# Kernel tuning notes

Measured on AMD Instinct MI355X. Metric: run time of the kernel, lower is better.

Reference implementation:

```python
import jax, jax.numpy as jnp
import numpy as np

EPS = 1e-06


def rotation_trick(e, q):
    # e, q: (..., D). Faithful to torch version, but r_rT @ e and
    # q_hat_e_hatT @ e are algebraically simplified to r*(r.e) and
    # q_hat*(e_hat.e), avoiding the (..., D, D) outer-product tensors.
    sg = jax.lax.stop_gradient
    e_norm = sg(jnp.linalg.norm(e, axis=-1, keepdims=True)) + EPS
    q_norm = sg(jnp.linalg.norm(q, axis=-1, keepdims=True)) + EPS
    e_hat = sg(e / e_norm)
    q_hat = sg(q / q_norm)
    lmbda = q_norm / e_norm
    r = e_hat + q_hat
    r = r / jnp.linalg.norm(r, axis=-1, keepdims=True)
    r_dot_e = jnp.sum(r * e, axis=-1, keepdims=True)
    ehat_dot_e = jnp.sum(e_hat * e, axis=-1, keepdims=True)
    return lmbda * (e - 2.0 * r * r_dot_e + 2.0 * q_hat * ehat_dot_e)


def setup_inputs() -> dict:
    key = jax.random.key(0)
    k1, k2 = jax.random.split(key)
    B, D, H, W = 8, 64, 32, 32
    K = 8192
    x = jax.random.normal(k1, (B, D, H, W), dtype=jnp.float32)
    # init_tensor: L2-normalize uniform rand along dim=1, scale=1
    e = jax.random.uniform(k2, (D, K), dtype=jnp.float32)
    e_i_ts = e / (jnp.linalg.norm(e, axis=1, keepdims=True) + 1e-12)
    return {"x": x, "e_i_ts": e_i_ts}


def reference(x, e_i_ts):
    # x: (B, D, H, W); e_i_ts: (D, K)
    B, D, H, W = x.shape
    x_perm = jnp.transpose(x, (0, 2, 3, 1))          # (B, H, W, D)
    flat_x = x_perm.reshape(-1, D)                   # (N, D)
    distances = (
        jnp.sum(flat_x**2, axis=1, keepdims=True)
        - 2.0 * flat_x @ e_i_ts
        + jnp.sum(e_i_ts**2, axis=0, keepdims=True)
    )                                                # (N, K)
    encoding_indices = jnp.argmin(distances, axis=1) # (N,)
    ind = encoding_indices.reshape(B, H, W)
    quantized_x = e_i_ts.T[ind]                      # (B, H, W, D) gather
    quantized_x_d = rotation_trick(x_perm, quantized_x)
    # permute back to channels-first
    q = jnp.transpose(quantized_x, (0, 3, 1, 2))
    q_d = jnp.transpose(quantized_x_d, (0, 3, 1, 2))
    return (q_d, q, ind)
```

## Files before the change

kernel.cpp:

```cpp
#include <hip/hip_runtime.h>
#include <float.h>
#include <math.h>

#define EPS 1e-6f

typedef __attribute__((ext_vector_type(8))) short short8;
typedef __attribute__((ext_vector_type(4))) float f32x4;

constexpr int Nn = 8192;
constexpr int Dd = 64;
constexpr int Kk = 8192;
constexpr int PLANE = Nn * Dd;
constexpr int KSPLIT = 16;
constexpr int KPB = Kk / KSPLIT;
constexpr int NT = KPB / 16;
constexpr int NPAIR = NT / 2;
constexpr int TILE_USH = 4096;
constexpr int PAIR_BYTES = 2 * TILE_USH * 2;

__device__ __forceinline__ void split3(float v, unsigned short& h1, unsigned short& h2, unsigned short& h3) {
    unsigned u = __float_as_uint(v);
    h1 = (unsigned short)(u >> 16);
    float r1 = v - __uint_as_float((unsigned)h1 << 16);
    h2 = (unsigned short)(__float_as_uint(r1) >> 16);
    float r2 = r1 - __uint_as_float((unsigned)h2 << 16);
    h3 = (unsigned short)(__float_as_uint(r2) >> 16);
}

__device__ __forceinline__ unsigned sortable(float v) {
    unsigned u = __float_as_uint(v);
    return (u & 0x80000000u) ? ~u : (u | 0x80000000u);
}
__device__ __forceinline__ float unsortable(unsigned s) {
    unsigned u = (s & 0x80000000u) ? (s & 0x7FFFFFFFu) : ~s;
    return __uint_as_float(u);
}

typedef __attribute__((address_space(3))) unsigned int lds_u32_t;
typedef __attribute__((address_space(1))) unsigned int glb_u32_t;
__device__ __forceinline__ void gload_lds16(const void* g, void* l) {
    __builtin_amdgcn_global_load_lds((const glb_u32_t*)g, (lds_u32_t*)l, 16, 0, 0);
}

__global__ __launch_bounds__(128) void prep_kernel(
    const float* __restrict__ e, const float* __restrict__ x,
    unsigned short* __restrict__ es_t, float* __restrict__ en2h,
    float* __restrict__ et,
    unsigned short* __restrict__ xs, float* __restrict__ xn2,
    unsigned long long* __restrict__ packed)
{
    const int tid = threadIdx.x;
    if (blockIdx.x < 64) {
        const int k = blockIdx.x * 128 + tid;
        const int t = k >> 4, l15 = k & 15;
        unsigned short* tb = es_t + (size_t)t * TILE_USH;
        float s = 0.f;
        #pragma unroll
        for (int c = 0; c < 8; ++c) {
            const int ks = c >> 2, kg = c & 3;
            short8 h1v, h2v, h3v;
            float fv[8];
            #pragma unroll
            for (int j = 0; j < 8; ++j) {
                float v = e[(c * 8 + j) * Kk + k];
                fv[j] = v;
                s = fmaf(v, v, s);
                unsigned short h1, h2, h3; split3(v, h1, h2, h3);
                h1v[j] = (short)h1; h2v[j] = (short)h2; h3v[j] = (short)h3;
            }
            const int lofs = (kg * 16 + l15) * 8;
            *(short8*)(tb + (0 * 2 + ks) * 512 + lofs) = h1v;
            *(short8*)(tb + (1 * 2 + ks) * 512 + lofs) = h2v;
            *(short8*)(tb + (2 * 2 + ks) * 512 + lofs) = h3v;
            *(float4*)(et + (size_t)k * Dd + c * 8)     = *(float4*)&fv[0];
            *(float4*)(et + (size_t)k * Dd + c * 8 + 4) = *(float4*)&fv[4];
        }
        unsigned short s1, s2, s3; split3(0.5f * s, s1, s2, s3);
        short8 env = {(short)s1, (short)s2, (short)s3, 0, 0, 0, 0, 0};
        short8 zz  = {0, 0, 0, 0, 0, 0, 0, 0};
        *(short8*)(tb + 6 * 512 + l15 * 8) = env;
        *(short8*)(tb + 6 * 512 + (16 + l15) * 8) = zz;
        *(short8*)(tb + 6 * 512 + (32 + l15) * 8) = zz;
        *(short8*)(tb + 6 * 512 + (48 + l15) * 8) = zz;
        en2h[k] = 0.5f * s;
    } else {
        const int p = (blockIdx.x - 64) * 128 + tid;
        const int b = p >> 10, hw = p & 1023;
        packed[p] = ~0ull;
        float s = 0.f;
        #pragma unroll
        for (int c = 0; c < 8; ++c) {
            short8 h1v, h2v, h3v;
            #pragma unroll
            for (int j = 0; j < 8; ++j) {
                float v = x[(b * Dd + c * 8 + j) * 1024 + hw];
                s = fmaf(v, v, s);
                unsigned short h1, h2, h3; split3(-v, h1, h2, h3);
                h1v[j] = (short)h1; h2v[j] = (short)h2; h3v[j] = (short)h3;
            }
            *(short8*)(xs + (size_t)p * Dd + c * 8) = h1v;
            *(short8*)(xs + PLANE + (size_t)p * Dd + c * 8) = h2v;
            *(short8*)(xs + 2 * PLANE + (size_t)p * Dd + c * 8) = h3v;
        }
        xn2[p] = s;
    }
}

__device__ __forceinline__ void tile_compute(
    const short8 (&a)[2][3][2], const short8 a_ones, const short8 (&b)[7],
    int nb, int l15, float (&bv)[2][4], int (&bi)[2][4])
{
    const f32x4 zero = {0.f, 0.f, 0.f, 0.f};
    f32x4 acc_en = __builtin_amdgcn_mfma_f32_16x16x32_bf16(a_ones, b[6], zero, 0, 0, 0);
    f32x4 acc[2][2];
    acc[0][0] = acc_en; acc[1][0] = acc_en;
    acc[0][1] = zero;   acc[1][1] = zero;
    #define PROD(sx, se) \
        acc[0][0] = __builtin_amdgcn_mfma_f32_16x16x32_bf16(a[0][sx][0], b[(se)*2+0], acc[0][0], 0,0,0); \
        acc[1][0] = __builtin_amdgcn_mfma_f32_16x16x32_bf16(a[1][sx][0], b[(se)*2+0], acc[1][0], 0,0,0); \
        acc[0][1] = __builtin_amdgcn_mfma_f32_16x16x32_bf16(a[0][sx][1], b[(se)*2+1], acc[0][1], 0,0,0); \
        acc[1][1] = __builtin_amdgcn_mfma_f32_16x16x32_bf16(a[1][sx][1], b[(se)*2+1], acc[1][1], 0,0,0);
    PROD(0,0) PROD(0,1) PROD(1,0) PROD(0,2) PROD(1,1) PROD(2,0)
    #undef PROD
    #pragma unroll
    for (int mi = 0; mi < 2; ++mi)
        #pragma unroll
        for (int j = 0; j < 4; ++j) {
            float s = acc[mi][0][j] + acc[mi][1][j];
            if (s < bv[mi][j]) { bv[mi][j] = s; bi[mi][j] = nb + l15; }
        }
}

__global__ __launch_bounds__(256, 2) void dist_mfma(
    const unsigned short* __restrict__ xs, const unsigned short* __restrict__ es_t,
    unsigned long long* __restrict__ packed)
{
    __shared__ __align__(16) unsigned short sB[2][2 * TILE_USH];

    const int tid = threadIdx.x;
    const int w = tid >> 6, lane = tid & 63;
    const int l15 = lane & 15, kg = lane >> 4;
    const int m0 = blockIdx.x * 128 + w * 32;
    const int t0 = blockIdx.y * NT;
    const int pr0 = t0 / 2;

    short8 a[2][3][2];
    #pragma unroll
    for (int mi = 0; mi < 2; ++mi) {
        const unsigned short* xp = xs + (size_t)(m0 + mi * 16 + l15) * Dd + kg * 8;
        #pragma unroll
        for (int s = 0; s < 3; ++s)
            #pragma unroll
            for (int ks = 0; ks < 2; ++ks)
                a[mi][s][ks] = *(const short8*)(xp + s * PLANE + ks * 32);
    }
    const short8 a_ones = (kg == 0)
        ? short8{(short)0x3F80, (short)0x3F80, (short)0x3F80, 0, 0, 0, 0, 0}
        : short8{0, 0, 0, 0, 0, 0, 0, 0};

    float bv[2][4]; int bi[2][4];
    #pragma unroll
    for (int mi = 0; mi < 2; ++mi)
        #pragma unroll
        for (int j = 0; j < 4; ++j) { bv[mi][j] = FLT_MAX; bi[mi][j] = 0; }

    #define STAGE_PAIR(buf, pi) { \
        const char* gb_ = (const char*)es_t + (size_t)(pi) * PAIR_BYTES; \
        char* lb_ = (char*)&sB[buf][0]; \
        _Pragma("unroll") \
        for (int r_ = 0; r_ < 4; ++r_) { \
            const int off_ = r_ * 4096 + w * 1024; \
            gload_lds16(gb_ + off_ + lane * 16, lb_ + off_); } }

    STAGE_PAIR(0, pr0)
    asm volatile("s_waitcnt vmcnt(0)" ::: "memory");
    asm volatile("s_barrier" ::: "memory");

    #pragma unroll 1
    for (int pp = 0; pp < NPAIR; ++pp) {
        const int cur = pp & 1;
        const int pn = (pp + 1 < NPAIR) ? pp + 1 : NPAIR - 1;
        STAGE_PAIR(cur ^ 1, pr0 + pn)
        asm volatile("s_waitcnt vmcnt(4)" ::: "memory");
        asm volatile("s_barrier" ::: "memory");

        short8 bf0[7], bf1[7];
        const unsigned short* lb = &sB[cur][lane * 8];
        #pragma unroll
        for (int f = 0; f < 7; ++f) bf0[f] = *(const short8*)(lb + f * 512);
        #pragma unroll
        for (int f = 0; f < 7; ++f) bf1[f] = *(const short8*)(lb + TILE_USH + f * 512);
        asm volatile("s_waitcnt lgkmcnt(0)" ::: "memory");
        asm volatile("s_barrier" ::: "memory");

        const int ti = t0 + pp * 2;
        tile_compute(a, a_ones, bf0, ti * 16, l15, bv, bi);
        tile_compute(a, a_ones, bf1, ti * 16 + 16, l15, bv, bi);
    }

    #pragma unroll
    for (int m = 1; m < 16; m <<= 1) {
        #pragma unroll
        for (int mi = 0; mi < 2; ++mi)
            #pragma unroll
            for (int j = 0; j < 4; ++j) {
                float ov = __shfl_xor(bv[mi][j], m, 64);
                int   oi = __shfl_xor(bi[mi][j], m, 64);
                if (ov < bv[mi][j] || (ov == bv[mi][j] && oi < bi[mi][j])) {
                    bv[mi][j] = ov; bi[mi][j] = oi;
                }
            }
    }
    if (l15 == 0) {
        #pragma unroll
        for (int mi = 0; mi < 2; ++mi)
            #pragma unroll
            for (int j = 0; j < 4; ++j) {
                int pix = m0 + mi * 16 + kg * 4 + j;
                unsigned long long pk =
                    ((unsigned long long)sortable(bv[mi][j]) << 32) | (unsigned)bi[mi][j];
                atomicMin(&packed[pix], pk);
            }
    }
}

__global__ __launch_bounds__(256) void apply_kernel(
    const float* __restrict__ x, const float* __restrict__ et,
    const float* __restrict__ en2h, const float* __restrict__ xn2,
    const unsigned long long* __restrict__ packed,
    float* __restrict__ out_qd, float* __restrict__ out_q, float* __restrict__ out_ind)
{
    const int p = blockIdx.x * 256 + threadIdx.x;
    const unsigned long long pk = packed[p];
    const int bii = (int)(pk & 0xFFFFFFFFu);
    const float bvv = unsortable((unsigned)(pk >> 32));
    if (blockIdx.y == 0) out_ind[p] = (float)bii;

    float sx2 = xn2[p];
    float enh = en2h[bii];
    float sq2 = 2.f * enh;
    float sxq = enh - bvv;
    float ne = sqrtf(sx2), nq = sqrtf(sq2);
    float inv_e = 1.f / (ne + EPS), inv_q = 1.f / (nq + EPS);
    float lmbda = (nq + EPS) * inv_e;
    float ehat_dot_e = sx2 * inv_e;
    float rn2 = sx2 * inv_e * inv_e + 2.f * sxq * inv_e * inv_q + sq2 * inv_q * inv_q;
    float inv_r = rsqrtf(rn2);
    float rde = (sx2 * inv_e + sxq * inv_q) * inv_r;
    float cx = lmbda * (1.f - 2.f * rde * inv_r * inv_e);
    float cq = 2.f * lmbda * inv_q * (ehat_dot_e - rde * inv_r);

    const int b = p >> 10, hw = p & 1023;
    const int d0 = blockIdx.y * 8;
    const float* xb = x + (b * Dd + d0) * 1024 + hw;
    const float* er = et + (size_t)bii * Dd + d0;
    float* qd_b = out_qd + (b * Dd + d0) * 1024 + hw;
    float* q_b  = out_q  + (b * Dd + d0) * 1024 + hw;
    #pragma unroll
    for (int dv = 0; dv < 2; ++dv) {
        float4 q4 = *(const float4*)(er + dv * 4);
        #pragma unroll
        for (int jj = 0; jj < 4; ++jj) {
            int d = dv * 4 + jj;
            float xv = xb[d * 1024];
            float qv = ((const float*)&q4)[jj];
            qd_b[d * 1024] = cx * xv + cq * qv;
            q_b[d * 1024]  = qv;
        }
    }
}

extern "C" void kernel_launch(void* const* d_in, const int* in_sizes, int n_in,
                              void* d_out, int out_size, void* d_ws, size_t ws_size,
                              hipStream_t stream) {
    const float* x = (const float*)d_in[0];
    const float* e = (const float*)d_in[1];
    float* out = (float*)d_out;
    float* out_qd  = out;
    float* out_q   = out + Nn * Dd;
    float* out_ind = out + 2 * Nn * Dd;

    unsigned short* xs   = (unsigned short*)d_ws;
    unsigned short* es_t = xs + 3 * PLANE;
    float* et   = (float*)(es_t + (size_t)(Kk / 16) * TILE_USH);
    float* en2h = et + (size_t)Kk * Dd;
    float* xn2  = en2h + Kk;
    unsigned long long* packed = (unsigned long long*)(xn2 + Nn);

    prep_kernel<<<128, 128, 0, stream>>>(e, x, es_t, en2h, et, xs, xn2, packed);
    dist_mfma<<<dim3(Nn / 128, KSPLIT), 256, 0, stream>>>(xs, es_t, packed);
    apply_kernel<<<dim3(Nn / 256, 8), 256, 0, stream>>>(x, et, en2h, xn2, packed,
                                                        out_qd, out_q, out_ind);
}
```

Before: 61.27 us.

## Register-block four M tiles per wave with per-wave LDS staging and no barriers

```diff
diff --git a/kernel.cpp b/kernel.cpp
--- a/kernel.cpp
+++ b/kernel.cpp
@@ -14,9 +14,7 @@
 constexpr int KSPLIT = 16;
 constexpr int KPB = Kk / KSPLIT;
 constexpr int NT = KPB / 16;
-constexpr int NPAIR = NT / 2;
-constexpr int TILE_USH = 4096;
-constexpr int PAIR_BYTES = 2 * TILE_USH * 2;
+constexpr int TILE_USH = 3072;
 
 __device__ __forceinline__ void split3(float v, unsigned short& h1, unsigned short& h2, unsigned short& h3) {
     unsigned u = __float_as_uint(v);
@@ -75,13 +73,6 @@
             *(float4*)(et + (size_t)k * Dd + c * 8)     = *(float4*)&fv[0];
             *(float4*)(et + (size_t)k * Dd + c * 8 + 4) = *(float4*)&fv[4];
         }
-        unsigned short s1, s2, s3; split3(0.5f * s, s1, s2, s3);
-        short8 env = {(short)s1, (short)s2, (short)s3, 0, 0, 0, 0, 0};
-        short8 zz  = {0, 0, 0, 0, 0, 0, 0, 0};
-        *(short8*)(tb + 6 * 512 + l15 * 8) = env;
-        *(short8*)(tb + 6 * 512 + (16 + l15) * 8) = zz;
-        *(short8*)(tb + 6 * 512 + (32 + l15) * 8) = zz;
-        *(short8*)(tb + 6 * 512 + (48 + l15) * 8) = zz;
         en2h[k] = 0.5f * s;
     } else {
         const int p = (blockIdx.x - 64) * 128 + tid;
@@ -107,23 +98,25 @@
 }
 
 __device__ __forceinline__ void tile_compute(
-    const short8 (&a)[2][3][2], const short8 a_ones, const short8 (&b)[7],
-    int nb, int l15, float (&bv)[2][4], int (&bi)[2][4])
-{
-    const f32x4 zero = {0.f, 0.f, 0.f, 0.f};
-    f32x4 acc_en = __builtin_amdgcn_mfma_f32_16x16x32_bf16(a_ones, b[6], zero, 0, 0, 0);
-    f32x4 acc[2][2];
-    acc[0][0] = acc_en; acc[1][0] = acc_en;
-    acc[0][1] = zero;   acc[1][1] = zero;
+    const short8 (&a)[4][3][2], const short8 (&b)[6], float en,
+    int nb, int l15, float (&bv)[4][4], int (&bi)[4][4])
+{
+    f32x4 acc[4][2];
+    #pragma unroll
+    for (int mi = 0; mi < 4; ++mi) {
+        acc[mi][0] = f32x4{en, en, en, en};
+        acc[mi][1] = f32x4{0.f, 0.f, 0.f, 0.f};
+    }
     #define PROD(sx, se) \
-        acc[0][0] = __builtin_amdgcn_mfma_f32_16x16x32_bf16(a[0][sx][0], b[(se)*2+0], acc[0][0], 0,0,0); \
-        acc[1][0] = __builtin_amdgcn_mfma_f32_16x16x32_bf16(a[1][sx][0], b[(se)*2+0], acc[1][0], 0,0,0); \
-        acc[0][1] = __builtin_amdgcn_mfma_f32_16x16x32_bf16(a[0][sx][1], b[(se)*2+1], acc[0][1], 0,0,0); \
-        acc[1][1] = __builtin_amdgcn_mfma_f32_16x16x32_bf16(a[1][sx][1], b[(se)*2+1], acc[1][1], 0,0,0);
+        _Pragma("unroll") \
+        for (int mi = 0; mi < 4; ++mi) { \
+            acc[mi][0] = __builtin_amdgcn_mfma_f32_16x16x32_bf16(a[mi][sx][0], b[(se)*2+0], acc[mi][0], 0,0,0); \
+            acc[mi][1] = __builtin_amdgcn_mfma_f32_16x16x32_bf16(a[mi][sx][1], b[(se)*2+1], acc[mi][1], 0,0,0); \
+        }
     PROD(0,0) PROD(0,1) PROD(1,0) PROD(0,2) PROD(1,1) PROD(2,0)
     #undef PROD
     #pragma unroll
-    for (int mi = 0; mi < 2; ++mi)
+    for (int mi = 0; mi < 4; ++mi)
         #pragma unroll
         for (int j = 0; j < 4; ++j) {
             float s = acc[mi][0][j] + acc[mi][1][j];
@@ -131,22 +124,23 @@
         }
 }
 
-__global__ __launch_bounds__(256, 2) void dist_mfma(
+__global__ __launch_bounds__(256, 1) void dist_mfma(
     const unsigned short* __restrict__ xs, const unsigned short* __restrict__ es_t,
+    const float* __restrict__ en2h,
     unsigned long long* __restrict__ packed)
 {
-    __shared__ __align__(16) unsigned short sB[2][2 * TILE_USH];
+    __shared__ __align__(16) unsigned short sW[4][2][TILE_USH];
 
     const int tid = threadIdx.x;
     const int w = tid >> 6, lane = tid & 63;
     const int l15 = lane & 15, kg = lane >> 4;
-    const int m0 = blockIdx.x * 128 + w * 32;
-    const int t0 = blockIdx.y * NT;
-    const int pr0 = t0 / 2;
-
-    short8 a[2][3][2];
-    #pragma unroll
-    for (int mi = 0; mi < 2; ++mi) {
+    const int m0 = blockIdx.x * 256 + w * 64;
+    const int tg0 = blockIdx.y * NT;
+    const int k0 = blockIdx.y * KPB;
+
+    short8 a[4][3][2];
+    #pragma unroll
+    for (int mi = 0; mi < 4; ++mi) {
         const unsigned short* xp = xs + (size_t)(m0 + mi * 16 + l15) * Dd + kg * 8;
         #pragma unroll
         for (int s = 0; s < 3; ++s)
@@ -154,54 +148,55 @@
             for (int ks = 0; ks < 2; ++ks)
                 a[mi][s][ks] = *(const short8*)(xp + s * PLANE + ks * 32);
     }
-    const short8 a_ones = (kg == 0)
-        ? short8{(short)0x3F80, (short)0x3F80, (short)0x3F80, 0, 0, 0, 0, 0}
-        : short8{0, 0, 0, 0, 0, 0, 0, 0};
-
-    float bv[2][4]; int bi[2][4];
-    #pragma unroll
-    for (int mi = 0; mi < 2; ++mi)
+
+    float bv[4][4]; int bi[4][4];
+    #pragma unroll
+    for (int mi = 0; mi < 4; ++mi)
         #pragma unroll
         for (int j = 0; j < 4; ++j) { bv[mi][j] = FLT_MAX; bi[mi][j] = 0; }
 
-    #define STAGE_PAIR(buf, pi) { \
-        const char* gb_ = (const char*)es_t + (size_t)(pi) * PAIR_BYTES; \
-        char* lb_ = (char*)&sB[buf][0]; \
+    #define STAGE_TILE(buf, ti) { \
+        const char* gb_ = (const char*)es_t + (size_t)(tg0 + (ti)) * (TILE_USH * 2); \
+        char* lb_ = (char*)&sW[w][buf][0]; \
         _Pragma("unroll") \
-        for (int r_ = 0; r_ < 4; ++r_) { \
-            const int off_ = r_ * 4096 + w * 1024; \
-            gload_lds16(gb_ + off_ + lane * 16, lb_ + off_); } }
-
-    STAGE_PAIR(0, pr0)
+        for (int r_ = 0; r_ < 6; ++r_) \
+            gload_lds16(gb_ + r_ * 1024 + lane * 16, lb_ + r_ * 1024); }
+
+    STAGE_TILE(0, 0)
+    float enA = en2h[k0 + l15];
+    float enB;
     asm volatile("s_waitcnt vmcnt(0)" ::: "memory");
-    asm volatile("s_barrier" ::: "memory");
 
     #pragma unroll 1
-    for (int pp = 0; pp < NPAIR; ++pp) {
-        const int cur = pp & 1;
-        const int pn = (pp + 1 < NPAIR) ? pp + 1 : NPAIR - 1;
-        STAGE_PAIR(cur ^ 1, pr0 + pn)
-        asm volatile("s_waitcnt vmcnt(4)" ::: "memory");
-        asm volatile("s_barrier" ::: "memory");
-
-        short8 bf0[7], bf1[7];
-        const unsigned short* lb = &sB[cur][lane * 8];
-        #pragma unroll
-        for (int f = 0; f < 7; ++f) bf0[f] = *(const short8*)(lb + f * 512);
-        #pragma unroll
-        for (int f = 0; f < 7; ++f) bf1[f] = *(const short8*)(lb + TILE_USH + f * 512);
-        asm volatile("s_waitcnt lgkmcnt(0)" ::: "memory");
-        asm volatile("s_barrier" ::: "memory");
-
-        const int ti = t0 + pp * 2;
-        tile_compute(a, a_ones, bf0, ti * 16, l15, bv, bi);
-        tile_compute(a, a_ones, bf1, ti * 16 + 16, l15, bv, bi);
+    for (int t = 0; t < NT; t += 2) {
+        {
+            const int pn = (t + 1 < NT) ? t + 1 : NT - 1;
+            STAGE_TILE(1, pn)
+            enB = en2h[k0 + pn * 16 + l15];
+            asm volatile("s_waitcnt vmcnt(7)" ::: "memory");
+            short8 bf[6];
+            const unsigned short* lb = &sW[w][0][lane * 8];
+            #pragma unroll
+            for (int f = 0; f < 6; ++f) bf[f] = *(const short8*)(lb + f * 512);
+            tile_compute(a, bf, enA, (tg0 + t) * 16, l15, bv, bi);
+        }
+        {
+            const int pn = (t + 2 < NT) ? t + 2 : NT - 1;
+            STAGE_TILE(0, pn)
+            enA = en2h[k0 + pn * 16 + l15];
+            asm volatile("s_waitcnt vmcnt(7)" ::: "memory");
+            short8 bf[6];
+            const unsigned short* lb = &sW[w][1][lane * 8];
+            #pragma unroll
+            for (int f = 0; f < 6; ++f) bf[f] = *(const short8*)(lb + f * 512);
+            tile_compute(a, bf, enB, (tg0 + t + 1) * 16, l15, bv, bi);
+        }
     }
 
     #pragma unroll
     for (int m = 1; m < 16; m <<= 1) {
         #pragma unroll
-        for (int mi = 0; mi < 2; ++mi)
+        for (int mi = 0; mi < 4; ++mi)
             #pragma unroll
             for (int j = 0; j < 4; ++j) {
                 float ov = __shfl_xor(bv[mi][j], m, 64);
@@ -213,7 +208,7 @@
     }
     if (l15 == 0) {
         #pragma unroll
-        for (int mi = 0; mi < 2; ++mi)
+        for (int mi = 0; mi < 4; ++mi)
             #pragma unroll
             for (int j = 0; j < 4; ++j) {
                 int pix = m0 + mi * 16 + kg * 4 + j;
@@ -288,7 +283,7 @@
     unsigned long long* packed = (unsigned long long*)(xn2 + Nn);
 
     prep_kernel<<<128, 128, 0, stream>>>(e, x, es_t, en2h, et, xs, xn2, packed);
-    dist_mfma<<<dim3(Nn / 128, KSPLIT), 256, 0, stream>>>(xs, es_t, packed);
+    dist_mfma<<<dim3(Nn / 256, KSPLIT), 256, 0, stream>>>(xs, es_t, en2h, packed);
     apply_kernel<<<dim3(Nn / 256, 8), 256, 0, stream>>>(x, et, en2h, xn2, packed,
                                                         out_qd, out_q, out_ind);
 }
```

Result: slower. 80.23 us (+31.0%).
